# Optimization experiments

Hardware: AMD Instinct MI355X
Metric: run time of the kernel (lower is better)

Reference implementation:

```python
import jax, jax.numpy as jnp
import numpy as np

V = 1000   # vocab_size
E = 1024   # encoder_output_dim
D = 512    # decoder_hidden_dim
A = 512    # attention_hidden_dim
T = 128    # token_embedding_size
B = 128    # batch
P = 196    # num_pix (14x14)
L = 257    # latex length -> 256 decode steps


def setup_inputs() -> dict:
    key = jax.random.key(0)
    ks = jax.random.split(key, 16)
    def p(k, shape, scale=0.05):
        return (jax.random.normal(k, shape, jnp.float32) * scale)
    return dict(
        features=jax.random.normal(ks[0], (B, P, E), jnp.float32),
        latexes=jax.random.randint(ks[1], (B, L), 0, V),
        emb=p(ks[2], (V, T)),
        Wenc=p(ks[3], (A, E)), benc=jnp.zeros((A,), jnp.float32),
        Wdec=p(ks[4], (A, D)), bdec=jnp.zeros((A,), jnp.float32),
        Wattn=p(ks[5], (1, A)), battn=jnp.zeros((1,), jnp.float32),
        W1ih=p(ks[6], (4 * D, E + T)), W1hh=p(ks[7], (4 * D, D)),
        b1ih=jnp.zeros((4 * D,), jnp.float32), b1hh=jnp.zeros((4 * D,), jnp.float32),
        W2ih=p(ks[8], (4 * D, D)), W2hh=p(ks[9], (4 * D, D)),
        b2ih=jnp.zeros((4 * D,), jnp.float32), b2hh=jnp.zeros((4 * D,), jnp.float32),
        Wh0=p(ks[10], (D, E)), bh0=jnp.zeros((D,), jnp.float32),
        Wc0=p(ks[11], (D, E)), bc0=jnp.zeros((D,), jnp.float32),
        Wg=p(ks[12], (E, D)), bg=jnp.zeros((E,), jnp.float32),
        Wf=p(ks[13], (V, D)), bf=jnp.zeros((V,), jnp.float32),
    )


def _lstm_cell(x, h, c, Wih, Whh, bih, bhh):
    # torch.nn.LSTMCell: gates order i, f, g, o
    g = x @ Wih.T + bih + h @ Whh.T + bhh
    i, f, gg, o = jnp.split(g, 4, axis=1)
    c_new = jax.nn.sigmoid(f) * c + jax.nn.sigmoid(i) * jnp.tanh(gg)
    h_new = jax.nn.sigmoid(o) * jnp.tanh(c_new)
    return h_new, c_new


def reference(features, latexes, emb, Wenc, benc, Wdec, bdec, Wattn, battn,
              W1ih, W1hh, b1ih, b1hh, W2ih, W2hh, b2ih, b2hh,
              Wh0, bh0, Wc0, bc0, Wg, bg, Wf, bf):
    seq_length = latexes.shape[1] - 1
    embeds = emb[latexes]                      # [B, L, T]
    mean_enc = features.mean(axis=1)           # [B, E]
    h1 = mean_enc @ Wh0.T + bh0
    c1 = mean_enc @ Wc0.T + bc0
    h2, c2 = h1, c1
    # encoder branch of attention is step-invariant; hoist out of the loop
    enc_t = features @ Wenc.T + benc           # [B, P, A]
    wa = Wattn[0]                              # [A]
    ba = battn[0]

    def step(carry, emb_s):
        h1, c1, h2, c2 = carry
        dec_t = h2 @ Wdec.T + bdec                         # [B, A]
        attn = jnp.tanh(enc_t + dec_t[:, None, :]) @ wa + ba  # [B, P]
        alpha = jax.nn.softmax(attn, axis=1)
        awe = jnp.einsum('bp,bpe->be', alpha, features)    # [B, E]
        x1 = jnp.concatenate([emb_s, awe], axis=1)         # [B, T+E]
        # NOTE: original computes gate = sigmoid(Wg h2 + bg) and multiplies the
        # attention encoding AFTER lstm1_input was built -> dead code; omitted.
        h1n, c1n = _lstm_cell(x1, h1, c1, W1ih, W1hh, b1ih, b1hh)
        h2n, c2n = _lstm_cell(h1n, h2, c2, W2ih, W2hh, b2ih, b2hh)
        out = h2n @ Wf.T + bf                              # [B, V]
        return (h1n, c1n, h2n, c2n), (out, alpha)

    emb_seq = jnp.swapaxes(embeds[:, :seq_length], 0, 1)   # [S, B, T]
    _, (preds, alphas) = jax.lax.scan(step, (h1, c1, h2, c2), emb_seq)
    preds = jnp.swapaxes(preds, 0, 1)                      # [B, S, V]
    alphas = jnp.swapaxes(alphas, 0, 1)                    # [B, S, P]
    return preds, alphas
```

## Files before the change

### kernel.cpp

```cpp
#include <hip/hip_runtime.h>
#include <hip/hip_bf16.h>
#include <stdint.h>

#define VV 1000
#define EE 1024
#define DD 512
#define AA 512
#define TT 128
#define BB 128
#define PP 196
#define SS 256

typedef unsigned short ushort_t;
typedef __attribute__((ext_vector_type(8))) short short8;
typedef __attribute__((ext_vector_type(4))) float floatx4;
typedef __attribute__((ext_vector_type(4))) unsigned short ushort4_t;
typedef __attribute__((ext_vector_type(8))) unsigned short ushort8_t;

__device__ __forceinline__ float bf2f(unsigned short h) {
    return __uint_as_float(((unsigned int)h) << 16);
}
__device__ __forceinline__ unsigned short f2bf(float x) {
    unsigned int u = __float_as_uint(x);
    unsigned int r = (u + 0x7fffu + ((u >> 16) & 1u)) >> 16;
    return (unsigned short)r;
}
__device__ __forceinline__ float sigmoidf_(float x) { return 1.f / (1.f + __expf(-x)); }
__device__ __forceinline__ float tanhf_(float x) {
    float e = __expf(2.f * x);
    return 1.f - 2.f / (e + 1.f);
}


__global__ void cvt_kernel(const float* __restrict__ src, ushort_t* __restrict__ dst, int n) {
    int i = blockIdx.x * 256 + threadIdx.x;
    if (i < n) dst[i] = f2bf(src[i]);
}

__global__ void mean_kernel(const float* __restrict__ feat, float* __restrict__ meanv) {
    int idx = blockIdx.x * 256 + threadIdx.x;
    int b = idx >> 10;
    int e = idx & 1023;
    const float* p = feat + (size_t)b * PP * 1024 + e;
    float s = 0.f;
    for (int pp = 0; pp < PP; ++pp) s += p[(size_t)pp * 1024];
    meanv[idx] = s * (1.f / 196.f);
}

__global__ __launch_bounds__(256) void init_kernel(
    const float* __restrict__ meanv, const float* __restrict__ Wh0, const float* __restrict__ bh0,
    const float* __restrict__ Wc0, const float* __restrict__ bc0,
    float* __restrict__ c1, float* __restrict__ c2,
    ushort_t* __restrict__ h1b, ushort_t* __restrict__ h2b) {
    int b = blockIdx.x, t = threadIdx.x;
    __shared__ float ml[1024];
    for (int i = t; i < 1024; i += 256) ml[i] = meanv[b * 1024 + i];
    __syncthreads();
    for (int d = t; d < 512; d += 256) {
        const float4* wh = (const float4*)(Wh0 + (size_t)d * 1024);
        const float4* wc = (const float4*)(Wc0 + (size_t)d * 1024);
        float ah = bh0[d], ac = bc0[d];
        #pragma unroll 4
        for (int j = 0; j < 256; ++j) {
            float4 w = wh[j];
            ah += w.x * ml[4 * j] + w.y * ml[4 * j + 1] + w.z * ml[4 * j + 2] + w.w * ml[4 * j + 3];
        }
        #pragma unroll 4
        for (int j = 0; j < 256; ++j) {
            float4 w = wc[j];
            ac += w.x * ml[4 * j] + w.y * ml[4 * j + 1] + w.z * ml[4 * j + 2] + w.w * ml[4 * j + 3];
        }
        c1[b * 512 + d] = ac;
        c2[b * 512 + d] = ac;
        ushort_t hb = f2bf(ah);
        h1b[b * 512 + d] = hb;
        h2b[b * 512 + d] = hb;
    }
}

__global__ __launch_bounds__(256) void enc_gemm(
    const ushort_t* __restrict__ feat_bf, const ushort_t* __restrict__ wenc_bf,
    const float* __restrict__ benc, ushort_t* __restrict__ enc_bf) {
    const int t = threadIdx.x, blk = blockIdx.x;
    const int bm = (blk % 392) * 64, bn = (blk / 392) * 64;
    const int lane = t & 63, wv = t >> 6;
    const int n = lane & 15, q = lane >> 4;
    const int arow = bm + wv * 16 + n;
    const short8* ap = (const short8*)(feat_bf + (size_t)arow * 1024 + q * 8);
    const short8* bp0 = (const short8*)(wenc_bf + (size_t)(bn + 0 * 16 + n) * 1024 + q * 8);
    const short8* bp1 = (const short8*)(wenc_bf + (size_t)(bn + 1 * 16 + n) * 1024 + q * 8);
    const short8* bp2 = (const short8*)(wenc_bf + (size_t)(bn + 2 * 16 + n) * 1024 + q * 8);
    const short8* bp3 = (const short8*)(wenc_bf + (size_t)(bn + 3 * 16 + n) * 1024 + q * 8);
    floatx4 acc0 = {0.f, 0.f, 0.f, 0.f}, acc1 = acc0, acc2 = acc0, acc3 = acc0;
    for (int ks = 0; ks < 32; ++ks) {
        short8 a8 = ap[ks * 4];
        acc0 = __builtin_amdgcn_mfma_f32_16x16x32_bf16(a8, bp0[ks * 4], acc0, 0, 0, 0);
        acc1 = __builtin_amdgcn_mfma_f32_16x16x32_bf16(a8, bp1[ks * 4], acc1, 0, 0, 0);
        acc2 = __builtin_amdgcn_mfma_f32_16x16x32_bf16(a8, bp2[ks * 4], acc2, 0, 0, 0);
        acc3 = __builtin_amdgcn_mfma_f32_16x16x32_bf16(a8, bp3[ks * 4], acc3, 0, 0, 0);
    }
    #pragma unroll
    for (int r = 0; r < 4; ++r) {
        int m = bm + wv * 16 + q * 4 + r;
        int a0 = bn + n;
        enc_bf[(size_t)m * 512 + a0] = f2bf(acc0[r] + benc[a0]);
        enc_bf[(size_t)m * 512 + a0 + 16] = f2bf(acc1[r] + benc[a0 + 16]);
        enc_bf[(size_t)m * 512 + a0 + 32] = f2bf(acc2[r] + benc[a0 + 32]);
        enc_bf[(size_t)m * 512 + a0 + 48] = f2bf(acc3[r] + benc[a0 + 48]);
    }
}


__global__ __launch_bounds__(256) void step_attn_preds(
    const ushort_t* __restrict__ enc_bf, const ushort_t* __restrict__ feat_bf,
    const ushort_t* __restrict__ wdec_bf, const ushort_t* __restrict__ wf_bf,
    const ushort_t* __restrict__ emb_bf, ushort_t* __restrict__ x1_bf,
    const ushort_t* __restrict__ h2cur, const int* __restrict__ latexes,
    const float* __restrict__ wattn, const float* __restrict__ battn,
    const float* __restrict__ bdec, const float* __restrict__ bfv,
    float* __restrict__ out, int s) {
    const int t = threadIdx.x;
    const int blk = blockIdx.x;
    if (blk < BB) {
        if (s >= SS) return;
        const int b = blk;
        __shared__ float dec_lds[512];
        __shared__ float wa_lds[512];
        __shared__ float h2row[512];
        __shared__ float red[256];
        __shared__ float attn_lds[256];
        __shared__ float alpha_lds[200];
        for (int i = t; i < 512; i += 256) {
            h2row[i] = bf2f(h2cur[b * 512 + i]);
            wa_lds[i] = wattn[i];
        }
        __syncthreads();
        for (int d = t; d < 512; d += 256) {
            const ushort8_t* wr = (const ushort8_t*)(wdec_bf + (size_t)d * 512);
            float acc = 0.f;
            #pragma unroll 4
            for (int j = 0; j < 64; ++j) {
                ushort8_t w8 = wr[j];
                const float* h8 = &h2row[j * 8];
                #pragma unroll
                for (int u = 0; u < 8; ++u) acc += bf2f(w8[u]) * h8[u];
            }
            dec_lds[d] = acc + bdec[d];
        }
        __syncthreads();
        const int wv = t >> 6, lane = t & 63;
        for (int p = wv; p < PP; p += 4) {
            const ushort8_t ev = *(const ushort8_t*)(enc_bf + ((size_t)(b * PP + p)) * 512 + lane * 8);
            float acc = 0.f;
            #pragma unroll
            for (int u = 0; u < 8; ++u) {
                float x = bf2f(ev[u]) + dec_lds[lane * 8 + u];
                acc += wa_lds[lane * 8 + u] * tanhf_(x);
            }
            #pragma unroll
            for (int off = 32; off > 0; off >>= 1) acc += __shfl_xor(acc, off, 64);
            if (lane == 0) attn_lds[p] = acc + battn[0];
        }
        __syncthreads();
        float logit = (t < PP) ? attn_lds[t] : -1e30f;
        red[t] = logit;
        __syncthreads();
        for (int st = 128; st > 0; st >>= 1) {
            if (t < st) red[t] = fmaxf(red[t], red[t + st]);
            __syncthreads();
        }
        float mx = red[0];
        __syncthreads();
        float e = (t < PP) ? __expf(logit - mx) : 0.f;
        red[t] = e;
        __syncthreads();
        for (int st = 128; st > 0; st >>= 1) {
            if (t < st) red[t] += red[t + st];
            __syncthreads();
        }
        float inv = 1.f / red[0];
        float a = e * inv;
        if (t < PP) {
            alpha_lds[t] = a;
            out[(size_t)32768000 + (size_t)b * 50176 + (size_t)s * 196 + t] = a;
        }
        __syncthreads();
        float a0 = 0.f, a1 = 0.f, a2 = 0.f, a3 = 0.f;
        const int e0 = t * 4;
        for (int p = 0; p < PP; ++p) {
            float av = alpha_lds[p];
            ushort4_t f4 = *(const ushort4_t*)(feat_bf + ((size_t)(b * PP + p)) * 1024 + e0);
            a0 += av * bf2f(f4[0]);
            a1 += av * bf2f(f4[1]);
            a2 += av * bf2f(f4[2]);
            a3 += av * bf2f(f4[3]);
        }
        ushort4_t o4;
        o4[0] = f2bf(a0); o4[1] = f2bf(a1); o4[2] = f2bf(a2); o4[3] = f2bf(a3);
        *(ushort4_t*)(x1_bf + (size_t)b * 1152 + 128 + e0) = o4;
        if (t < TT) {
            int tok = latexes[b * 257 + s];
            x1_bf[(size_t)b * 1152 + t] = emb_bf[tok * TT + t];
        }
    } else {
        if (s == 0) return;
        const int wg2 = blk - BB;
        const int v0 = wg2 * 16;
        const int lane = t & 63, wv = t >> 6;
        const int n = lane & 15, q = lane >> 4;
        const int vrow = v0 + n;
        const int vclamp = vrow < VV ? vrow : VV - 1;
        const short8* bp = (const short8*)(wf_bf + (size_t)vclamp * 512 + q * 8);
        const int m0 = 2 * wv * 16 + n;
        const short8* ap0 = (const short8*)(h2cur + (size_t)m0 * 512 + q * 8);
        const short8* ap1 = (const short8*)(h2cur + (size_t)(m0 + 16) * 512 + q * 8);
        floatx4 acc0 = {0.f, 0.f, 0.f, 0.f}, acc1 = acc0;
        for (int ks = 0; ks < 16; ++ks) {
            short8 b8 = bp[ks * 4];
            acc0 = __builtin_amdgcn_mfma_f32_16x16x32_bf16(ap0[ks * 4], b8, acc0, 0, 0, 0);
            acc1 = __builtin_amdgcn_mfma_f32_16x16x32_bf16(ap1[ks * 4], b8, acc1, 0, 0, 0);
        }
        if (vrow < VV) {
            float cb = bfv[vrow];
            size_t so = (size_t)(s - 1) * 1000 + vrow;
            #pragma unroll
            for (int r = 0; r < 4; ++r) {
                int br = 2 * wv * 16 + q * 4 + r;
                out[(size_t)br * 256000 + so] = acc0[r] + cb;
                out[(size_t)(br + 16) * 256000 + so] = acc1[r] + cb;
            }
        }
    }
}

__global__ __launch_bounds__(256) void lstm_cell_kernel(
    const ushort_t* __restrict__ A1, int k1, const ushort_t* __restrict__ Wih,
    const ushort_t* __restrict__ A2, const ushort_t* __restrict__ Whh,
    const float* __restrict__ bih, const float* __restrict__ bhh,
    float* __restrict__ cst, ushort_t* __restrict__ hout) {
    const int t = threadIdx.x, wg = blockIdx.x;
    const int d0 = wg * 4;
    const int lane = t & 63, wv = t >> 6;
    const int n = lane & 15, q = lane >> 4;
    const int col = (n >> 2) * 512 + d0 + (n & 3);
    const int m0 = 2 * wv * 16 + n;
    floatx4 acc0 = {0.f, 0.f, 0.f, 0.f}, acc1 = acc0;
    {
        const short8* bp = (const short8*)(Wih + (size_t)col * k1 + q * 8);
        const short8* a0 = (const short8*)(A1 + (size_t)m0 * k1 + q * 8);
        const short8* a1 = (const short8*)(A1 + (size_t)(m0 + 16) * k1 + q * 8);
        const int nk = k1 >> 5;
        for (int ks = 0; ks < nk; ++ks) {
            short8 b8 = bp[ks * 4];
            acc0 = __builtin_amdgcn_mfma_f32_16x16x32_bf16(a0[ks * 4], b8, acc0, 0, 0, 0);
            acc1 = __builtin_amdgcn_mfma_f32_16x16x32_bf16(a1[ks * 4], b8, acc1, 0, 0, 0);
        }
    }
    {
        const short8* bp = (const short8*)(Whh + (size_t)col * 512 + q * 8);
        const short8* a0 = (const short8*)(A2 + (size_t)m0 * 512 + q * 8);
        const short8* a1 = (const short8*)(A2 + (size_t)(m0 + 16) * 512 + q * 8);
        for (int ks = 0; ks < 16; ++ks) {
            short8 b8 = bp[ks * 4];
            acc0 = __builtin_amdgcn_mfma_f32_16x16x32_bf16(a0[ks * 4], b8, acc0, 0, 0, 0);
            acc1 = __builtin_amdgcn_mfma_f32_16x16x32_bf16(a1[ks * 4], b8, acc1, 0, 0, 0);
        }
    }
    __shared__ float glds[128][16];
    #pragma unroll
    for (int r = 0; r < 4; ++r) {
        glds[2 * wv * 16 + q * 4 + r][n] = acc0[r];
        glds[2 * wv * 16 + 16 + q * 4 + r][n] = acc1[r];
    }
    __syncthreads();
    for (int idx = t; idx < 512; idx += 256) {
        int bb = idx >> 2, dj = idx & 3;
        int d = d0 + dj;
        float gi = glds[bb][dj] + bih[d] + bhh[d];
        float gf = glds[bb][4 + dj] + bih[512 + d] + bhh[512 + d];
        float gg = glds[bb][8 + dj] + bih[1024 + d] + bhh[1024 + d];
        float go = glds[bb][12 + dj] + bih[1536 + d] + bhh[1536 + d];
        float co = cst[bb * 512 + d];
        float cn = sigmoidf_(gf) * co + sigmoidf_(gi) * tanhf_(gg);
        float hn = sigmoidf_(go) * tanhf_(cn);
        cst[bb * 512 + d] = cn;
        hout[bb * 512 + d] = f2bf(hn);
    }
}

extern "C" void kernel_launch(void* const* d_in, const int* in_sizes, int n_in,
                              void* d_out, int out_size, void* d_ws, size_t ws_size,
                              hipStream_t stream) {
    const float* features = (const float*)d_in[0];
    const int* latexes = (const int*)d_in[1];
    const float* emb = (const float*)d_in[2];
    const float* Wenc = (const float*)d_in[3];
    const float* benc = (const float*)d_in[4];
    const float* Wdec = (const float*)d_in[5];
    const float* bdec = (const float*)d_in[6];
    const float* Wattn = (const float*)d_in[7];
    const float* battn = (const float*)d_in[8];
    const float* W1ih = (const float*)d_in[9];
    const float* W1hh = (const float*)d_in[10];
    const float* b1ih = (const float*)d_in[11];
    const float* b1hh = (const float*)d_in[12];
    const float* W2ih = (const float*)d_in[13];
    const float* W2hh = (const float*)d_in[14];
    const float* b2ih = (const float*)d_in[15];
    const float* b2hh = (const float*)d_in[16];
    const float* Wh0 = (const float*)d_in[17];
    const float* bh0 = (const float*)d_in[18];
    const float* Wc0 = (const float*)d_in[19];
    const float* bc0 = (const float*)d_in[20];
    const float* Wf = (const float*)d_in[23];
    const float* bfv = (const float*)d_in[24];
    float* out = (float*)d_out;

    char* ws = (char*)d_ws;
    size_t off = 0;
    auto alloc = [&](size_t bytes) {
        void* p = ws + off;
        off += (bytes + 255) & ~(size_t)255;
        return p;
    };
    ushort_t* feat_bf = (ushort_t*)alloc(25690112ull * 2);
    ushort_t* enc_bf = (ushort_t*)alloc(12845056ull * 2);
    ushort_t* w1ih_bf = (ushort_t*)alloc(2359296ull * 2);
    ushort_t* w1hh_bf = (ushort_t*)alloc(1048576ull * 2);
    ushort_t* w2ih_bf = (ushort_t*)alloc(1048576ull * 2);
    ushort_t* w2hh_bf = (ushort_t*)alloc(1048576ull * 2);
    ushort_t* wf_bf = (ushort_t*)alloc(512000ull * 2);
    ushort_t* wdec_bf = (ushort_t*)alloc(262144ull * 2);
    ushort_t* wenc_bf = (ushort_t*)alloc(524288ull * 2);
    ushort_t* emb_bf = (ushort_t*)alloc(128000ull * 2);
    float* meanv = (float*)alloc(131072ull * 4);
    float* c1 = (float*)alloc(65536ull * 4);
    float* c2 = (float*)alloc(65536ull * 4);
    ushort_t* h1b0 = (ushort_t*)alloc(65536ull * 2);
    ushort_t* h1b1 = (ushort_t*)alloc(65536ull * 2);
    ushort_t* h2b0 = (ushort_t*)alloc(65536ull * 2);
    ushort_t* h2b1 = (ushort_t*)alloc(65536ull * 2);
    ushort_t* x1_bf = (ushort_t*)alloc(147456ull * 2);
    ushort_t* h1b[2] = {h1b0, h1b1};
    ushort_t* h2b[2] = {h2b0, h2b1};

    auto cv = [&](const float* s, ushort_t* d, int n) {
        cvt_kernel<<<(n + 255) / 256, 256, 0, stream>>>(s, d, n);
    };
    cv(features, feat_bf, 25690112);
    cv(Wenc, wenc_bf, 524288);
    cv(W1ih, w1ih_bf, 2359296);
    cv(W1hh, w1hh_bf, 1048576);
    cv(W2ih, w2ih_bf, 1048576);
    cv(W2hh, w2hh_bf, 1048576);
    cv(Wf, wf_bf, 512000);
    cv(Wdec, wdec_bf, 262144);
    cv(emb, emb_bf, 128000);
    mean_kernel<<<512, 256, 0, stream>>>(features, meanv);
    init_kernel<<<128, 256, 0, stream>>>(meanv, Wh0, bh0, Wc0, bc0, c1, c2, h1b[0], h2b[0]);
    enc_gemm<<<3136, 256, 0, stream>>>(feat_bf, wenc_bf, benc, enc_bf);

    for (int s = 0; s <= SS; ++s) {
        int cur = s & 1, nxt = 1 - cur;
        step_attn_preds<<<191, 256, 0, stream>>>(enc_bf, feat_bf, wdec_bf, wf_bf, emb_bf, x1_bf,
                                                 h2b[cur], latexes, Wattn, battn, bdec, bfv, out, s);
        if (s < SS) {
            lstm_cell_kernel<<<128, 256, 0, stream>>>(x1_bf, 1152, w1ih_bf, h1b[cur], w1hh_bf,
                                                      b1ih, b1hh, c1, h1b[nxt]);
            lstm_cell_kernel<<<128, 256, 0, stream>>>(h1b[nxt], 512, w2ih_bf, h2b[cur], w2hh_bf,
                                                      b2ih, b2hh, c2, h2b[nxt]);
        }
    }
}
```

Measured before the change: 27.88 ms.

## Fuse per-step decode launches into one persistent kernel with grid barriers

```diff
diff --git a/kernel.cpp b/kernel.cpp
--- a/kernel.cpp
+++ b/kernel.cpp
@@ -1,5 +1,4 @@
 #include <hip/hip_runtime.h>
-#include <hip/hip_bf16.h>
 #include <stdint.h>
 
 #define VV 1000
@@ -25,16 +24,31 @@
     unsigned int r = (u + 0x7fffu + ((u >> 16) & 1u)) >> 16;
     return (unsigned short)r;
 }
-__device__ __forceinline__ float sigmoidf_(float x) { return 1.f / (1.f + __expf(-x)); }
+__device__ __forceinline__ float fast_rcp(float x) { return __builtin_amdgcn_rcpf(x); }
+__device__ __forceinline__ float sigmoidf_(float x) { return fast_rcp(1.f + __expf(-x)); }
 __device__ __forceinline__ float tanhf_(float x) {
     float e = __expf(2.f * x);
-    return 1.f - 2.f / (e + 1.f);
+    return 1.f - 2.f * fast_rcp(e + 1.f);
+}
+
+template <int NKS>
+__device__ __forceinline__ floatx4 mmK(const short8* __restrict__ ap,
+                                       const short8* __restrict__ bp, floatx4 acc) {
+#pragma unroll
+    for (int ks = 0; ks < NKS; ++ks)
+        acc = __builtin_amdgcn_mfma_f32_16x16x32_bf16(ap[ks * 4], bp[ks * 4], acc, 0, 0, 0);
+    return acc;
 }
 
 
 __global__ void cvt_kernel(const float* __restrict__ src, ushort_t* __restrict__ dst, int n) {
     int i = blockIdx.x * 256 + threadIdx.x;
     if (i < n) dst[i] = f2bf(src[i]);
+}
+
+__global__ void zero_kernel(int* __restrict__ p, int n) {
+    int i = blockIdx.x * 256 + threadIdx.x;
+    if (i < n) p[i] = 0;
 }
 
 __global__ void mean_kernel(const float* __restrict__ feat, float* __restrict__ meanv) {
@@ -110,181 +124,221 @@
     }
 }
 
-
-__global__ __launch_bounds__(256) void step_attn_preds(
-    const ushort_t* __restrict__ enc_bf, const ushort_t* __restrict__ feat_bf,
-    const ushort_t* __restrict__ wdec_bf, const ushort_t* __restrict__ wf_bf,
-    const ushort_t* __restrict__ emb_bf, ushort_t* __restrict__ x1_bf,
-    const ushort_t* __restrict__ h2cur, const int* __restrict__ latexes,
-    const float* __restrict__ wattn, const float* __restrict__ battn,
-    const float* __restrict__ bdec, const float* __restrict__ bfv,
-    float* __restrict__ out, int s) {
-    const int t = threadIdx.x;
-    const int blk = blockIdx.x;
-    if (blk < BB) {
-        if (s >= SS) return;
-        const int b = blk;
-        __shared__ float dec_lds[512];
-        __shared__ float wa_lds[512];
-        __shared__ float h2row[512];
-        __shared__ float red[256];
-        __shared__ float attn_lds[256];
-        __shared__ float alpha_lds[200];
-        for (int i = t; i < 512; i += 256) {
-            h2row[i] = bf2f(h2cur[b * 512 + i]);
-            wa_lds[i] = wattn[i];
-        }
-        __syncthreads();
-        for (int d = t; d < 512; d += 256) {
-            const ushort8_t* wr = (const ushort8_t*)(wdec_bf + (size_t)d * 512);
-            float acc = 0.f;
-            #pragma unroll 4
-            for (int j = 0; j < 64; ++j) {
-                ushort8_t w8 = wr[j];
-                const float* h8 = &h2row[j * 8];
-                #pragma unroll
-                for (int u = 0; u < 8; ++u) acc += bf2f(w8[u]) * h8[u];
-            }
-            dec_lds[d] = acc + bdec[d];
-        }
-        __syncthreads();
-        const int wv = t >> 6, lane = t & 63;
-        for (int p = wv; p < PP; p += 4) {
-            const ushort8_t ev = *(const ushort8_t*)(enc_bf + ((size_t)(b * PP + p)) * 512 + lane * 8);
-            float acc = 0.f;
-            #pragma unroll
-            for (int u = 0; u < 8; ++u) {
-                float x = bf2f(ev[u]) + dec_lds[lane * 8 + u];
-                acc += wa_lds[lane * 8 + u] * tanhf_(x);
-            }
-            #pragma unroll
-            for (int off = 32; off > 0; off >>= 1) acc += __shfl_xor(acc, off, 64);
-            if (lane == 0) attn_lds[p] = acc + battn[0];
-        }
-        __syncthreads();
-        float logit = (t < PP) ? attn_lds[t] : -1e30f;
-        red[t] = logit;
-        __syncthreads();
-        for (int st = 128; st > 0; st >>= 1) {
-            if (t < st) red[t] = fmaxf(red[t], red[t + st]);
-            __syncthreads();
-        }
-        float mx = red[0];
-        __syncthreads();
-        float e = (t < PP) ? __expf(logit - mx) : 0.f;
-        red[t] = e;
-        __syncthreads();
-        for (int st = 128; st > 0; st >>= 1) {
-            if (t < st) red[t] += red[t + st];
-            __syncthreads();
-        }
-        float inv = 1.f / red[0];
-        float a = e * inv;
-        if (t < PP) {
-            alpha_lds[t] = a;
-            out[(size_t)32768000 + (size_t)b * 50176 + (size_t)s * 196 + t] = a;
-        }
-        __syncthreads();
-        float a0 = 0.f, a1 = 0.f, a2 = 0.f, a3 = 0.f;
-        const int e0 = t * 4;
-        for (int p = 0; p < PP; ++p) {
-            float av = alpha_lds[p];
-            ushort4_t f4 = *(const ushort4_t*)(feat_bf + ((size_t)(b * PP + p)) * 1024 + e0);
-            a0 += av * bf2f(f4[0]);
-            a1 += av * bf2f(f4[1]);
-            a2 += av * bf2f(f4[2]);
-            a3 += av * bf2f(f4[3]);
-        }
-        ushort4_t o4;
-        o4[0] = f2bf(a0); o4[1] = f2bf(a1); o4[2] = f2bf(a2); o4[3] = f2bf(a3);
-        *(ushort4_t*)(x1_bf + (size_t)b * 1152 + 128 + e0) = o4;
-        if (t < TT) {
-            int tok = latexes[b * 257 + s];
-            x1_bf[(size_t)b * 1152 + t] = emb_bf[tok * TT + t];
-        }
-    } else {
-        if (s == 0) return;
-        const int wg2 = blk - BB;
-        const int v0 = wg2 * 16;
-        const int lane = t & 63, wv = t >> 6;
-        const int n = lane & 15, q = lane >> 4;
-        const int vrow = v0 + n;
-        const int vclamp = vrow < VV ? vrow : VV - 1;
-        const short8* bp = (const short8*)(wf_bf + (size_t)vclamp * 512 + q * 8);
-        const int m0 = 2 * wv * 16 + n;
-        const short8* ap0 = (const short8*)(h2cur + (size_t)m0 * 512 + q * 8);
-        const short8* ap1 = (const short8*)(h2cur + (size_t)(m0 + 16) * 512 + q * 8);
-        floatx4 acc0 = {0.f, 0.f, 0.f, 0.f}, acc1 = acc0;
-        for (int ks = 0; ks < 16; ++ks) {
-            short8 b8 = bp[ks * 4];
-            acc0 = __builtin_amdgcn_mfma_f32_16x16x32_bf16(ap0[ks * 4], b8, acc0, 0, 0, 0);
-            acc1 = __builtin_amdgcn_mfma_f32_16x16x32_bf16(ap1[ks * 4], b8, acc1, 0, 0, 0);
-        }
-        if (vrow < VV) {
-            float cb = bfv[vrow];
-            size_t so = (size_t)(s - 1) * 1000 + vrow;
-            #pragma unroll
-            for (int r = 0; r < 4; ++r) {
-                int br = 2 * wv * 16 + q * 4 + r;
-                out[(size_t)br * 256000 + so] = acc0[r] + cb;
-                out[(size_t)(br + 16) * 256000 + so] = acc1[r] + cb;
-            }
-        }
-    }
-}
-
-__global__ __launch_bounds__(256) void lstm_cell_kernel(
+__device__ __forceinline__ void gbar(int* __restrict__ bar, int k) {
+    __syncthreads();
+    if (threadIdx.x == 0) {
+        __threadfence();
+        int* grp = bar + (blockIdx.x >> 5) * 32;
+        int old = __hip_atomic_fetch_add(grp, 1, __ATOMIC_ACQ_REL, __HIP_MEMORY_SCOPE_AGENT);
+        if (old + 1 == 32 * k) {
+            int r = __hip_atomic_fetch_add(bar + 256, 1, __ATOMIC_ACQ_REL, __HIP_MEMORY_SCOPE_AGENT);
+            if (r + 1 == 8 * k) {
+                __hip_atomic_store(bar + 288, k, __ATOMIC_RELEASE, __HIP_MEMORY_SCOPE_AGENT);
+            }
+        }
+        while (__hip_atomic_load(bar + 288, __ATOMIC_ACQUIRE, __HIP_MEMORY_SCOPE_AGENT) < k) {
+            __builtin_amdgcn_s_sleep(2);
+        }
+        __threadfence();
+    }
+    __syncthreads();
+}
+
+__device__ __forceinline__ void preds_tile(int w2, int s, const ushort_t* __restrict__ h2cur,
+                                           const ushort_t* __restrict__ wf_bf,
+                                           const float* __restrict__ bfv,
+                                           float* __restrict__ out, int wv, int n, int q) {
+    const int v0 = (w2 >> 1) * 16;
+    const int m0 = (w2 & 1) * 64 + wv * 16;
+    const int vrow = v0 + n;
+    const int vc = vrow < VV ? vrow : VV - 1;
+    const short8* bp = (const short8*)(wf_bf + (size_t)vc * 512 + q * 8);
+    const short8* ap = (const short8*)(h2cur + (size_t)(m0 + n) * 512 + q * 8);
+    floatx4 acc0 = {0.f, 0.f, 0.f, 0.f}, acc1 = acc0;
+    acc0 = mmK<8>(ap, bp, acc0);
+    acc1 = mmK<8>(ap + 32, bp + 32, acc1);
+    acc0 += acc1;
+    if (vrow < VV) {
+        const float cb = bfv[vrow];
+        const size_t so = (size_t)(s - 1) * 1000 + vrow;
+        #pragma unroll
+        for (int r = 0; r < 4; ++r)
+            out[(size_t)(m0 + q * 4 + r) * 256000 + so] = acc0[r] + cb;
+    }
+}
+
+__device__ __forceinline__ void lstm_phase(
+    int wg, int t, int wv, int n, int q,
     const ushort_t* __restrict__ A1, int k1, const ushort_t* __restrict__ Wih,
-    const ushort_t* __restrict__ A2, const ushort_t* __restrict__ Whh,
+    const ushort_t* __restrict__ A2v, const ushort_t* __restrict__ Whh,
     const float* __restrict__ bih, const float* __restrict__ bhh,
-    float* __restrict__ cst, ushort_t* __restrict__ hout) {
-    const int t = threadIdx.x, wg = blockIdx.x;
-    const int d0 = wg * 4;
-    const int lane = t & 63, wv = t >> 6;
-    const int n = lane & 15, q = lane >> 4;
+    float* __restrict__ cst, ushort_t* __restrict__ hout, float (*glds)[17]) {
+    const int rh = wg >> 7, d0 = (wg & 127) * 4;
     const int col = (n >> 2) * 512 + d0 + (n & 3);
-    const int m0 = 2 * wv * 16 + n;
+    const int m0 = rh * 64 + wv * 16;
     floatx4 acc0 = {0.f, 0.f, 0.f, 0.f}, acc1 = acc0;
     {
         const short8* bp = (const short8*)(Wih + (size_t)col * k1 + q * 8);
-        const short8* a0 = (const short8*)(A1 + (size_t)m0 * k1 + q * 8);
-        const short8* a1 = (const short8*)(A1 + (size_t)(m0 + 16) * k1 + q * 8);
-        const int nk = k1 >> 5;
-        for (int ks = 0; ks < nk; ++ks) {
-            short8 b8 = bp[ks * 4];
-            acc0 = __builtin_amdgcn_mfma_f32_16x16x32_bf16(a0[ks * 4], b8, acc0, 0, 0, 0);
-            acc1 = __builtin_amdgcn_mfma_f32_16x16x32_bf16(a1[ks * 4], b8, acc1, 0, 0, 0);
+        const short8* ap = (const short8*)(A1 + (size_t)(m0 + n) * k1 + q * 8);
+        if (k1 == 1152) {
+            acc0 = mmK<18>(ap, bp, acc0);
+            acc1 = mmK<18>(ap + 72, bp + 72, acc1);
+        } else {
+            acc0 = mmK<8>(ap, bp, acc0);
+            acc1 = mmK<8>(ap + 32, bp + 32, acc1);
         }
     }
     {
         const short8* bp = (const short8*)(Whh + (size_t)col * 512 + q * 8);
-        const short8* a0 = (const short8*)(A2 + (size_t)m0 * 512 + q * 8);
-        const short8* a1 = (const short8*)(A2 + (size_t)(m0 + 16) * 512 + q * 8);
-        for (int ks = 0; ks < 16; ++ks) {
-            short8 b8 = bp[ks * 4];
-            acc0 = __builtin_amdgcn_mfma_f32_16x16x32_bf16(a0[ks * 4], b8, acc0, 0, 0, 0);
-            acc1 = __builtin_amdgcn_mfma_f32_16x16x32_bf16(a1[ks * 4], b8, acc1, 0, 0, 0);
-        }
-    }
-    __shared__ float glds[128][16];
+        const short8* ap = (const short8*)(A2v + (size_t)(m0 + n) * 512 + q * 8);
+        acc0 = mmK<8>(ap, bp, acc0);
+        acc1 = mmK<8>(ap + 32, bp + 32, acc1);
+    }
+    acc0 += acc1;
     #pragma unroll
-    for (int r = 0; r < 4; ++r) {
-        glds[2 * wv * 16 + q * 4 + r][n] = acc0[r];
-        glds[2 * wv * 16 + 16 + q * 4 + r][n] = acc1[r];
-    }
+    for (int r = 0; r < 4; ++r) glds[wv * 16 + q * 4 + r][n] = acc0[r];
     __syncthreads();
-    for (int idx = t; idx < 512; idx += 256) {
-        int bb = idx >> 2, dj = idx & 3;
-        int d = d0 + dj;
-        float gi = glds[bb][dj] + bih[d] + bhh[d];
-        float gf = glds[bb][4 + dj] + bih[512 + d] + bhh[512 + d];
-        float gg = glds[bb][8 + dj] + bih[1024 + d] + bhh[1024 + d];
-        float go = glds[bb][12 + dj] + bih[1536 + d] + bhh[1536 + d];
-        float co = cst[bb * 512 + d];
-        float cn = sigmoidf_(gf) * co + sigmoidf_(gi) * tanhf_(gg);
-        float hn = sigmoidf_(go) * tanhf_(cn);
-        cst[bb * 512 + d] = cn;
-        hout[bb * 512 + d] = f2bf(hn);
+    const int bl = t >> 2, dj = t & 3;
+    const int d = d0 + dj;
+    const int b = rh * 64 + bl;
+    float gi = glds[bl][dj] + bih[d] + bhh[d];
+    float gf = glds[bl][4 + dj] + bih[512 + d] + bhh[512 + d];
+    float gg = glds[bl][8 + dj] + bih[1024 + d] + bhh[1024 + d];
+    float go = glds[bl][12 + dj] + bih[1536 + d] + bhh[1536 + d];
+    float co = cst[b * 512 + d];
+    float cn = sigmoidf_(gf) * co + sigmoidf_(gi) * tanhf_(gg);
+    float hn = sigmoidf_(go) * tanhf_(cn);
+    cst[b * 512 + d] = cn;
+    hout[b * 512 + d] = f2bf(hn);
+}
+
+__global__ __launch_bounds__(256, 1) void decode_loop(
+    const ushort_t* __restrict__ enc_bf, const ushort_t* __restrict__ feat_bf,
+    const ushort_t* __restrict__ wdec_bf, const ushort_t* __restrict__ wf_bf,
+    const ushort_t* __restrict__ emb_bf,
+    const ushort_t* __restrict__ w1ih_bf, const ushort_t* __restrict__ w1hh_bf,
+    const ushort_t* __restrict__ w2ih_bf, const ushort_t* __restrict__ w2hh_bf,
+    const int* __restrict__ latexes,
+    const float* __restrict__ wattn, const float* __restrict__ battn,
+    const float* __restrict__ bdec, const float* __restrict__ bfv,
+    const float* __restrict__ b1ih, const float* __restrict__ b1hh,
+    const float* __restrict__ b2ih, const float* __restrict__ b2hh,
+    float* __restrict__ c1, float* __restrict__ c2,
+    ushort_t* __restrict__ h1b0, ushort_t* __restrict__ h1b1,
+    ushort_t* __restrict__ h2b0, ushort_t* __restrict__ h2b1,
+    ushort_t* __restrict__ x1_bf, float* __restrict__ decb,
+    float* __restrict__ out, int* __restrict__ bar) {
+    const int wg = blockIdx.x, t = threadIdx.x;
+    const int lane = t & 63, wv = t >> 6;
+    const int n = lane & 15, q = lane >> 4;
+
+    __shared__ float wa_lds[512];
+    __shared__ float dec_lds[512];
+    __shared__ float red[256];
+    __shared__ float attn_lds[200];
+    __shared__ float alpha_lds[200];
+    __shared__ float glds[64][17];
+
+    for (int i = t; i < 512; i += 256) wa_lds[i] = wattn[i];
+
+    int bc = 0;
+    for (int s = 0;; ++s) {
+        const ushort_t* h1cur = (s & 1) ? h1b1 : h1b0;
+        const ushort_t* h2cur = (s & 1) ? h2b1 : h2b0;
+        ushort_t* h1nxt = (s & 1) ? h1b0 : h1b1;
+        ushort_t* h2nxt = (s & 1) ? h2b0 : h2b1;
+
+        if (wg < 64 && s < SS) {
+            const int n0 = (wg >> 1) * 16;
+            const int m0 = (wg & 1) * 64 + wv * 16;
+            const short8* ap = (const short8*)(h2cur + (size_t)(m0 + n) * 512 + q * 8);
+            const short8* bp = (const short8*)(wdec_bf + (size_t)(n0 + n) * 512 + q * 8);
+            floatx4 acc0 = {0.f, 0.f, 0.f, 0.f}, acc1 = acc0;
+            acc0 = mmK<8>(ap, bp, acc0);
+            acc1 = mmK<8>(ap + 32, bp + 32, acc1);
+            acc0 += acc1;
+            const float cb = bdec[n0 + n];
+            #pragma unroll
+            for (int r = 0; r < 4; ++r)
+                decb[(size_t)(m0 + q * 4 + r) * 512 + n0 + n] = acc0[r] + cb;
+        }
+        if (s == SS) {
+            if (wg >= 128 && wg < 254) preds_tile(wg - 128, SS, h2cur, wf_bf, bfv, out, wv, n, q);
+            break;
+        }
+        gbar(bar, ++bc);
+
+        if (wg < BB) {
+            const int b = wg;
+            if (t < TT) {
+                int tok = latexes[b * 257 + s];
+                x1_bf[(size_t)b * 1152 + t] = emb_bf[tok * TT + t];
+            }
+            for (int i = t; i < 512; i += 256) dec_lds[i] = decb[b * 512 + i];
+            __syncthreads();
+            const float ba = battn[0];
+            for (int p = wv; p < PP; p += 4) {
+                const ushort8_t ev =
+                    *(const ushort8_t*)(enc_bf + ((size_t)(b * PP + p)) * 512 + lane * 8);
+                float acc = 0.f;
+                #pragma unroll
+                for (int u = 0; u < 8; ++u) {
+                    float x = bf2f(ev[u]) + dec_lds[lane * 8 + u];
+                    acc += wa_lds[lane * 8 + u] * tanhf_(x);
+                }
+                #pragma unroll
+                for (int off = 32; off > 0; off >>= 1) acc += __shfl_xor(acc, off, 64);
+                if (lane == 0) attn_lds[p] = acc + ba;
+            }
+            __syncthreads();
+            float logit = (t < PP) ? attn_lds[t] : -1e30f;
+            red[t] = logit;
+            __syncthreads();
+            for (int st = 128; st > 0; st >>= 1) {
+                if (t < st) red[t] = fmaxf(red[t], red[t + st]);
+                __syncthreads();
+            }
+            float mx = red[0];
+            __syncthreads();
+            float e = (t < PP) ? __expf(logit - mx) : 0.f;
+            red[t] = e;
+            __syncthreads();
+            for (int st = 128; st > 0; st >>= 1) {
+                if (t < st) red[t] += red[t + st];
+                __syncthreads();
+            }
+            float inv = 1.f / red[0];
+            float a = e * inv;
+            if (t < PP) {
+                alpha_lds[t] = a;
+                out[(size_t)32768000 + (size_t)b * 50176 + (size_t)s * 196 + t] = a;
+            }
+            __syncthreads();
+            float a0 = 0.f, a1 = 0.f, a2 = 0.f, a3 = 0.f;
+            const int e0 = t * 4;
+            for (int p = 0; p < PP; ++p) {
+                float av = alpha_lds[p];
+                ushort4_t f4 = *(const ushort4_t*)(feat_bf + ((size_t)(b * PP + p)) * 1024 + e0);
+                a0 += av * bf2f(f4[0]);
+                a1 += av * bf2f(f4[1]);
+                a2 += av * bf2f(f4[2]);
+                a3 += av * bf2f(f4[3]);
+            }
+            ushort4_t o4;
+            o4[0] = f2bf(a0); o4[1] = f2bf(a1); o4[2] = f2bf(a2); o4[3] = f2bf(a3);
+            *(ushort4_t*)(x1_bf + (size_t)b * 1152 + TT + e0) = o4;
+        } else if (wg >= 128 && wg < 254 && s > 0) {
+            preds_tile(wg - 128, s, h2cur, wf_bf, bfv, out, wv, n, q);
+        }
+        gbar(bar, ++bc);
+
+        lstm_phase(wg, t, wv, n, q, x1_bf, 1152, w1ih_bf, h1cur, w1hh_bf,
+                   b1ih, b1hh, c1, h1nxt, glds);
+        gbar(bar, ++bc);
+
+        lstm_phase(wg, t, wv, n, q, h1nxt, 512, w2ih_bf, h2cur, w2hh_bf,
+                   b2ih, b2hh, c2, h2nxt, glds);
+        gbar(bar, ++bc);
     }
 }
 
@@ -341,8 +395,8 @@
     ushort_t* h2b0 = (ushort_t*)alloc(65536ull * 2);
     ushort_t* h2b1 = (ushort_t*)alloc(65536ull * 2);
     ushort_t* x1_bf = (ushort_t*)alloc(147456ull * 2);
-    ushort_t* h1b[2] = {h1b0, h1b1};
-    ushort_t* h2b[2] = {h2b0, h2b1};
+    float* decb = (float*)alloc(65536ull * 4);
+    int* bar = (int*)alloc(512 * sizeof(int));
 
     auto cv = [&](const float* s, ushort_t* d, int n) {
         cvt_kernel<<<(n + 255) / 256, 256, 0, stream>>>(s, d, n);
@@ -356,19 +410,13 @@
     cv(Wf, wf_bf, 512000);
     cv(Wdec, wdec_bf, 262144);
     cv(emb, emb_bf, 128000);
+    zero_kernel<<<2, 256, 0, stream>>>(bar, 512);
     mean_kernel<<<512, 256, 0, stream>>>(features, meanv);
-    init_kernel<<<128, 256, 0, stream>>>(meanv, Wh0, bh0, Wc0, bc0, c1, c2, h1b[0], h2b[0]);
+    init_kernel<<<128, 256, 0, stream>>>(meanv, Wh0, bh0, Wc0, bc0, c1, c2, h1b0, h2b0);
     enc_gemm<<<3136, 256, 0, stream>>>(feat_bf, wenc_bf, benc, enc_bf);
 
-    for (int s = 0; s <= SS; ++s) {
-        int cur = s & 1, nxt = 1 - cur;
-        step_attn_preds<<<191, 256, 0, stream>>>(enc_bf, feat_bf, wdec_bf, wf_bf, emb_bf, x1_bf,
-                                                 h2b[cur], latexes, Wattn, battn, bdec, bfv, out, s);
-        if (s < SS) {
-            lstm_cell_kernel<<<128, 256, 0, stream>>>(x1_bf, 1152, w1ih_bf, h1b[cur], w1hh_bf,
-                                                      b1ih, b1hh, c1, h1b[nxt]);
-            lstm_cell_kernel<<<128, 256, 0, stream>>>(h1b[nxt], 512, w2ih_bf, h2b[cur], w2hh_bf,
-                                                      b2ih, b2hh, c2, h2b[nxt]);
-        }
-    }
-}
+    decode_loop<<<256, 256, 0, stream>>>(
+        enc_bf, feat_bf, wdec_bf, wf_bf, emb_bf, w1ih_bf, w1hh_bf, w2ih_bf, w2hh_bf,
+        latexes, Wattn, battn, bdec, bfv, b1ih, b1hh, b2ih, b2hh,
+        c1, c2, h1b0, h1b1, h2b0, h2b1, x1_bf, decb, out, bar);
+}
```

After: 64.04 ms. 2.3x slower.
